# Performance work log

Measured on AMD Instinct MI355X. Metric: run time of the kernel, lower is better.

## Reference

```python
import jax, jax.numpy as jnp
import numpy as np
import math

B, T, D, H = 2, 2048, 1024, 16
HD = D // H


def setup_inputs() -> dict:
    key = jax.random.key(0)
    k1, k2, k3 = jax.random.split(key, 3)
    x = jax.random.normal(k1, (B, T, D), dtype=jnp.float32)
    # weights scaled like typical init to keep activations sane
    w_qkv = jax.random.normal(k2, (D, 3 * D), dtype=jnp.float32) / math.sqrt(D)
    w_out = jax.random.normal(k3, (D, D), dtype=jnp.float32) / math.sqrt(D)
    return {"x": x, "w_qkv": w_qkv, "w_out": w_out}


def reference(x, w_qkv, w_out):
    b, t, d = x.shape
    h, hd = H, HD
    qkv = x @ w_qkv                                # (b, t, 3d)
    qkv = qkv.reshape(b, t, h, 3 * hd).transpose(0, 2, 1, 3)  # (b, h, t, 3hd)
    q, k, v = jnp.split(qkv, 3, axis=-1)           # each (b, h, t, hd)
    scaled = jnp.einsum('bhqd,bhkd->bhqk', q, k) / math.sqrt(hd)
    # causal mask: strictly upper triangle -> -inf (as in torch.triu(full(-inf),1))
    causal = jnp.tril(jnp.ones((t, t), dtype=bool))
    scaled = jnp.where(causal, scaled, -jnp.inf)
    attn = jax.nn.softmax(scaled, axis=-1)
    vals = jnp.einsum('bhqk,bhkd->bhqd', attn, v)  # (b, h, t, hd)
    # NOTE: original reshapes (b,h,t,hd)->(b,t,h*hd) WITHOUT permuting heads back.
    vals = vals.reshape(b, t, h * hd)
    return vals @ w_out
```

## Files before the change

### kernel.cpp

```cpp
#include <hip/hip_runtime.h>
#include <hip/hip_bf16.h>
#include <math.h>

#define BB 2
#define TT 2048
#define DD 1024
#define HH 16
#define HDD 64

typedef __attribute__((ext_vector_type(8))) short short8;
typedef __attribute__((ext_vector_type(4))) float f32x4;

__device__ __forceinline__ short f2bf(float f) {
  __hip_bfloat16 h = __float2bfloat16(f);
  return *reinterpret_cast<short*>(&h);
}

__device__ __forceinline__ float bf2f(short s) {
  unsigned u = ((unsigned)(unsigned short)s) << 16;
  return __builtin_bit_cast(float, u);
}

__device__ __forceinline__ void gload_lds16(const void* g, void* l) {
  __builtin_amdgcn_global_load_lds(
      (const __attribute__((address_space(1))) unsigned int*)g,
      (__attribute__((address_space(3))) unsigned int*)l, 16, 0, 0);
}

__global__ __launch_bounds__(256) void cvt_f32_bf16(
    const float* __restrict__ in, short* __restrict__ out, int n8) {
  int i = blockIdx.x * 256 + threadIdx.x;
  if (i >= n8) return;
  const float4* p = (const float4*)in + (size_t)i * 2;
  float4 a = p[0], b = p[1];
  short8 o;
  o[0] = f2bf(a.x); o[1] = f2bf(a.y); o[2] = f2bf(a.z); o[3] = f2bf(a.w);
  o[4] = f2bf(b.x); o[5] = f2bf(b.y); o[6] = f2bf(b.z); o[7] = f2bf(b.w);
  *((short8*)out + i) = o;
}

__global__ __launch_bounds__(256) void transpose_f32_bf16(
    const float* __restrict__ W, short* __restrict__ WT, int R, int C) {
  __shared__ float tile[32][33];
  const int c0 = blockIdx.x * 32, r0 = blockIdx.y * 32;
  const int tx = threadIdx.x & 31, ty = threadIdx.x >> 5;
#pragma unroll
  for (int i = 0; i < 32; i += 8)
    tile[ty + i][tx] = W[(size_t)(r0 + ty + i) * C + c0 + tx];
  __syncthreads();
#pragma unroll
  for (int i = 0; i < 32; i += 8)
    WT[(size_t)(c0 + ty + i) * R + r0 + tx] = f2bf(tile[tx][ty + i]);
}

__global__ __launch_bounds__(256) void vtrans(const short* __restrict__ qkv,
                                              short* __restrict__ vtg) {
  const int t0 = blockIdx.x * 64;
  const int h = blockIdx.y, b = blockIdx.z;
  __shared__ __align__(16) short sm[64 * 64];
  const int tid = threadIdx.x;
  const short* Vg = qkv + (size_t)(b * TT) * 3072 + h * 192 + 128;
#pragma unroll
  for (int r2 = 0; r2 < 2; ++r2) {
    int c = tid + r2 * 256;
    int t = c >> 3, d0 = (c & 7) * 8;
    short8 v = *(const short8*)(Vg + (size_t)(t0 + t) * 3072 + d0);
#pragma unroll
    for (int j = 0; j < 8; ++j) {
      int d = d0 + j;
      int byte = (d << 7) + ((t * 2) ^ (((d >> 3) & 7) << 4));
      *(short*)((char*)sm + byte) = v[j];
    }
  }
  __syncthreads();
  short* outp = vtg + (size_t)(b * HH + h) * HDD * TT + t0;
#pragma unroll
  for (int r2 = 0; r2 < 2; ++r2) {
    int c = tid + r2 * 256;
    int d = c >> 3, tc = c & 7;
    int byte = (d << 7) + ((tc ^ ((d >> 3) & 7)) << 4);
    short8 v = *(const short8*)((char*)sm + byte);
    *(short8*)(outp + (size_t)d * TT + tc * 8) = v;
  }
}

template <bool OUT_BF16>
__global__ __launch_bounds__(256) void gemm_bf16_mfma(
    const short* __restrict__ A, const short* __restrict__ BT,
    void* __restrict__ Cv, int M, int N, int K) {
  constexpr int BM = 128, BN = 128, BK = 64;
  __shared__ __align__(16) short As[BM * BK];
  __shared__ __align__(16) short Bs[BN * BK];

  const int nbx = N / BN;
  const int nwg = nbx * (M / BM);
  int bid = blockIdx.x;
  {
    int q = nwg >> 3;
    bid = (bid & 7) * q + (bid >> 3);
  }
  const int m0 = (bid / nbx) * BM;
  const int n0 = (bid % nbx) * BN;

  const int tid = threadIdx.x;
  const int lane = tid & 63;
  const int l15 = lane & 15;
  const int g4 = lane >> 4;
  const int wm = tid >> 7;
  const int wn = (tid >> 6) & 1;
  const int swz = (l15 & 7) << 4;

  f32x4 acc[4][4];
#pragma unroll
  for (int i = 0; i < 4; ++i)
#pragma unroll
    for (int j = 0; j < 4; ++j) acc[i][j] = (f32x4){0.f, 0.f, 0.f, 0.f};

  for (int k0 = 0; k0 < K; k0 += BK) {
    __syncthreads();
#pragma unroll
    for (int r = 0; r < 4; ++r) {
      int c = tid + r * 256;
      int row = c >> 3, cc = c & 7;
      int sc = (cc ^ (row & 7)) * 8;
      gload_lds16(A + (size_t)(m0 + row) * K + k0 + sc, (char*)As + c * 16);
    }
#pragma unroll
    for (int r = 0; r < 4; ++r) {
      int c = tid + r * 256;
      int row = c >> 3, cc = c & 7;
      int sc = (cc ^ (row & 7)) * 8;
      gload_lds16(BT + (size_t)(n0 + row) * K + k0 + sc, (char*)Bs + c * 16);
    }
    __syncthreads();

#pragma unroll
    for (int kk = 0; kk < 2; ++kk) {
      short8 af[4], bfr[4];
#pragma unroll
      for (int i = 0; i < 4; ++i) {
        int row = wm * 64 + i * 16 + l15;
        af[i] = *(const short8*)((const char*)As + row * 128 +
                                 (((kk * 4 + g4) << 4) ^ swz));
      }
#pragma unroll
      for (int j = 0; j < 4; ++j) {
        int row = wn * 64 + j * 16 + l15;
        bfr[j] = *(const short8*)((const char*)Bs + row * 128 +
                                  (((kk * 4 + g4) << 4) ^ swz));
      }
#pragma unroll
      for (int i = 0; i < 4; ++i)
#pragma unroll
        for (int j = 0; j < 4; ++j)
          acc[i][j] = __builtin_amdgcn_mfma_f32_16x16x32_bf16(
              af[i], bfr[j], acc[i][j], 0, 0, 0);
    }
  }

#pragma unroll
  for (int i = 0; i < 4; ++i) {
#pragma unroll
    for (int j = 0; j < 4; ++j) {
#pragma unroll
      for (int r = 0; r < 4; ++r) {
        size_t idx = (size_t)(m0 + wm * 64 + i * 16 + g4 * 4 + r) * N +
                     n0 + wn * 64 + j * 16 + l15;
        if (OUT_BF16)
          ((short*)Cv)[idx] = f2bf(acc[i][j][r]);
        else
          ((float*)Cv)[idx] = acc[i][j][r];
      }
    }
  }
}

__global__ __launch_bounds__(256) void attn_flash4(
    const short* __restrict__ qkv, const short* __restrict__ vtg,
    short* __restrict__ vals, char* __restrict__ parts,
    float* __restrict__ mldiag) {
  const int bid = blockIdx.x;
  const int xcd = bid & 7;
  const int j   = bid >> 3;
  const int g   = xcd + ((j & 3) << 3);
  const int c   = 79 - (j >> 2);
  int qt, ci, cnt;
  if (c < 8)       { qt = c;                          ci = 0;      cnt = 1; }
  else if (c < 24) { int u = c - 8;  qt = 8 + (u >> 1);  ci = u & 1;  cnt = 2; }
  else if (c < 48) { int u = c - 24; qt = 16 + u / 3;    ci = u % 3;  cnt = 3; }
  else             { int u = c - 48; qt = 24 + (u >> 2); ci = u & 3;  cnt = 4; }
  const int h = g & 15, b = g >> 4;
  const int nt  = qt + 1;
  const int it0 = ci * 8;
  const int it1 = min(it0 + 8, nt);

  const int tid = threadIdx.x;
  const int w = tid >> 6, lane = tid & 63, l15 = lane & 15, g4 = lane >> 4;

  __shared__ __align__(16) short Ks[2][64 * 64];
  __shared__ __align__(16) short Vs[2][64 * 64];
  __shared__ __align__(16) short Ps[4 * 16 * 64];

  const size_t bhbase = (size_t)(b * TT) * 3072 + (size_t)h * 192;
  char* const pswb = (char*)Ps + w * 2048;

  const float MFIX = 12.0f;
  const float SSC = 0.18033688011112042f;

  const int c2 = tid + 256;
  const int r1 = tid >> 3, s1 = tid & 7;
  const int r2 = c2 >> 3,  s2 = c2 & 7;
  const size_t kgo1 = (size_t)r1 * 3072 + ((s1 ^ (r1 & 7)) * 8);
  const size_t kgo2 = (size_t)r2 * 3072 + ((s2 ^ (r2 & 7)) * 8);
  const size_t vgo1 = (size_t)r1 * TT + ((s1 ^ (r1 & 7)) * 8);
  const size_t vgo2 = (size_t)r2 * TT + ((s2 ^ (r2 & 7)) * 8);
  char* const ldsK0 = (char*)Ks[0] + tid * 16;
  char* const ldsK1 = (char*)Ks[1] + tid * 16;
  char* const ldsV0 = (char*)Vs[0] + tid * 16;
  char* const ldsV1 = (char*)Vs[1] + tid * 16;

  const short* kptr = qkv + bhbase + 64 + (size_t)(it0 * 64) * 3072;
  const short* vptr = vtg + (size_t)(b * HH + h) * HDD * TT + it0 * 64;

  auto STAGE = [&](int buf) {
    char* kl = buf ? ldsK1 : ldsK0;
    char* vl = buf ? ldsV1 : ldsV0;
    gload_lds16(kptr + kgo1, kl);
    gload_lds16(kptr + kgo2, kl + 4096);
    gload_lds16(vptr + vgo1, vl);
    gload_lds16(vptr + vgo2, vl + 4096);
    kptr += 64 * 3072;
    vptr += 64;
  };

  short8 qf0, qf1;
  {
    const int qrow = qt * 64 + w * 16 + l15;
    const short* Qp = qkv + bhbase + (size_t)qrow * 3072 + g4 * 8;
    short8 q0 = *(const short8*)(Qp);
    short8 q1 = *(const short8*)(Qp + 32);
#pragma unroll
    for (int jj = 0; jj < 8; ++jj) {
      qf0[jj] = f2bf(bf2f(q0[jj]) * SSC);
      qf1[jj] = f2bf(bf2f(q1[jj]) * SSC);
    }
  }

  float lsum = 0.f;
  f32x4 oacc[4];
#pragma unroll
  for (int dt = 0; dt < 4; ++dt) oacc[dt] = (f32x4){0.f, 0.f, 0.f, 0.f};

  STAGE(0);
  int cur = 0;

  const int pxor = (l15 & 3) << 1;
  const int sw = l15 & 7;

#pragma unroll 1
  for (int it = it0; it < it1; ++it) {
    __syncthreads();
    if (it + 1 < it1) STAGE(cur ^ 1);

    const char* ksb = cur ? (const char*)Ks[1] : (const char*)Ks[0];
    const char* vsb = cur ? (const char*)Vs[1] : (const char*)Vs[0];

    f32x4 s4[4];
    __builtin_amdgcn_s_setprio(1);
#pragma unroll
    for (int kt = 0; kt < 4; ++kt) {
      const char* kb = ksb + (kt * 16 + l15) * 128;
      short8 kf0 = *(const short8*)(kb + ((g4 ^ sw) << 4));
      short8 kf1 = *(const short8*)(kb + (((g4 + 4) ^ sw) << 4));
      s4[kt] = (f32x4){0.f, 0.f, 0.f, 0.f};
      s4[kt] = __builtin_amdgcn_mfma_f32_16x16x32_bf16(kf0, qf0, s4[kt], 0, 0, 0);
      s4[kt] = __builtin_amdgcn_mfma_f32_16x16x32_bf16(kf1, qf1, s4[kt], 0, 0, 0);
    }
    __builtin_amdgcn_s_setprio(0);

    if (it == qt) {
      const int qg = w * 16 + l15;
#pragma unroll
      for (int kt = 0; kt < 4; ++kt) {
#pragma unroll
        for (int r = 0; r < 4; ++r) {
          int kg = kt * 16 + g4 * 4 + r;
          if (kg > qg) s4[kt][r] = -INFINITY;
        }
      }
    }

    float p[4][4];
    float ts = 0.f;
#pragma unroll
    for (int kt = 0; kt < 4; ++kt)
#pragma unroll
      for (int r = 0; r < 4; ++r) {
        float e = exp2f(s4[kt][r] - MFIX);
        p[kt][r] = e;
        ts += e;
      }
    lsum += ts;

#pragma unroll
    for (int kt = 0; kt < 4; ++kt) {
      unsigned lo, hi;
      asm("v_cvt_pk_bf16_f32 %0, %1, %2" : "=v"(lo) : "v"(p[kt][0]), "v"(p[kt][1]));
      asm("v_cvt_pk_bf16_f32 %0, %1, %2" : "=v"(hi) : "v"(p[kt][2]), "v"(p[kt][3]));
      int slot = 2 * kt + (g4 >> 1);
      *(uint2*)(pswb + l15 * 128 + ((slot ^ pxor) << 4) + ((g4 & 1) << 3)) =
          make_uint2(lo, hi);
    }
    short8 pa0 = *(const short8*)(pswb + l15 * 128 + ((g4 ^ pxor) << 4));
    short8 pa1 = *(const short8*)(pswb + l15 * 128 + (((4 + g4) ^ pxor) << 4));

    __builtin_amdgcn_s_setprio(1);
#pragma unroll
    for (int dt = 0; dt < 4; ++dt) {
      const char* vb = vsb + (dt * 16 + l15) * 128;
      short8 vb0 = *(const short8*)(vb + ((g4 ^ sw) << 4));
      short8 vb1 = *(const short8*)(vb + (((g4 + 4) ^ sw) << 4));
      oacc[dt] = __builtin_amdgcn_mfma_f32_16x16x32_bf16(pa0, vb0, oacc[dt], 0, 0, 0);
      oacc[dt] = __builtin_amdgcn_mfma_f32_16x16x32_bf16(pa1, vb1, oacc[dt], 0, 0, 0);
    }
    __builtin_amdgcn_s_setprio(0);

    cur ^= 1;
  }

  lsum += __shfl_xor(lsum, 16);
  lsum += __shfl_xor(lsum, 32);

  if (cnt == 1) {
    float inv = 1.f / lsum;
    float invq[4];
#pragma unroll
    for (int r = 0; r < 4; ++r) invq[r] = __shfl(inv, g4 * 4 + r, 16);
#pragma unroll
    for (int r = 0; r < 4; ++r) {
      int qglob = qt * 64 + w * 16 + g4 * 4 + r;
      size_t rowbase = (((size_t)b * HH + h) * TT + qglob) * HDD;
#pragma unroll
      for (int dt = 0; dt < 4; ++dt)
        vals[rowbase + dt * 16 + l15] = f2bf(oacc[dt][r] * invq[r]);
    }
  } else if (ci == cnt - 1) {
#pragma unroll
    for (int r = 0; r < 4; ++r) {
      int qglob = qt * 64 + w * 16 + g4 * 4 + r;
      size_t rowbase = (((size_t)b * HH + h) * TT + qglob) * HDD;
#pragma unroll
      for (int dt = 0; dt < 4; ++dt)
        vals[rowbase + dt * 16 + l15] = f2bf(oacc[dt][r]);
    }
    if (g4 == 0) {
      int qtglob = g * 32 + qt;
      int qrow = w * 16 + l15;
      mldiag[qtglob * 128 + qrow] = MFIX;
      mldiag[qtglob * 128 + 64 + qrow] = lsum;
    }
  } else {
    int pl = (qt < 16) ? (qt - 8)
             : (qt < 24 ? 8 + (qt - 16) * 2 : 24 + (qt - 24) * 3);
    char* pp = parts + (size_t)(g * 48 + pl + ci) * 8704;
    short* po = (short*)pp;
#pragma unroll
    for (int r = 0; r < 4; ++r)
#pragma unroll
      for (int dt = 0; dt < 4; ++dt)
        po[(w * 16 + g4 * 4 + r) * 64 + dt * 16 + l15] = f2bf(oacc[dt][r]);
    if (g4 == 0) {
      int qrow = w * 16 + l15;
      *(float*)(pp + 8192 + qrow * 4) = MFIX;
      *(float*)(pp + 8448 + qrow * 4) = lsum;
    }
  }
}

__global__ __launch_bounds__(256) void attn_merge(
    short* __restrict__ vals, const char* __restrict__ parts,
    const float* __restrict__ mldiag) {
  const int qt = 8 + blockIdx.x;
  const int g  = blockIdx.y;
  const int tid = threadIdx.x;
  const int q  = tid >> 2;
  const int dq = (tid & 3) * 16;
  const int np = qt < 16 ? 1 : (qt < 24 ? 2 : 3);
  const int pl = (qt < 16) ? (qt - 8)
                 : (qt < 24 ? 8 + (qt - 16) * 2 : 24 + (qt - 24) * 3);
  const int qtglob = g * 32 + qt;
  const char* pbase = parts + (size_t)(g * 48 + pl) * 8704;

  float mdiag = mldiag[qtglob * 128 + q];
  float ldiag = mldiag[qtglob * 128 + 64 + q];

  float mstar = mdiag;
  for (int p = 0; p < np; ++p)
    mstar = fmaxf(mstar, *(const float*)(pbase + (size_t)p * 8704 + 8192 + q * 4));

  size_t vbase = ((size_t)g * TT + qt * 64 + q) * HDD + dq;
  float o[16];
  {
    float wd = exp2f(mdiag - mstar);
    short8 a = *(const short8*)(vals + vbase);
    short8 bb = *(const short8*)(vals + vbase + 8);
#pragma unroll
    for (int jj = 0; jj < 8; ++jj) {
      o[jj] = bf2f(a[jj]) * wd;
      o[8 + jj] = bf2f(bb[jj]) * wd;
    }
    ldiag *= wd;
  }
  float lacc = ldiag;
  for (int p = 0; p < np; ++p) {
    const char* pp = pbase + (size_t)p * 8704;
    float wp = exp2f(*(const float*)(pp + 8192 + q * 4) - mstar);
    lacc += *(const float*)(pp + 8448 + q * 4) * wp;
    const short* po = (const short*)pp + q * 64 + dq;
    short8 a = *(const short8*)po;
    short8 bb = *(const short8*)(po + 8);
#pragma unroll
    for (int jj = 0; jj < 8; ++jj) {
      o[jj] += bf2f(a[jj]) * wp;
      o[8 + jj] += bf2f(bb[jj]) * wp;
    }
  }
  float inv = 1.f / lacc;
  short8 oa, ob;
#pragma unroll
  for (int jj = 0; jj < 8; ++jj) {
    oa[jj] = f2bf(o[jj] * inv);
    ob[jj] = f2bf(o[8 + jj] * inv);
  }
  *(short8*)(vals + vbase) = oa;
  *(short8*)(vals + vbase + 8) = ob;
}

extern "C" void kernel_launch(void* const* d_in, const int* in_sizes, int n_in,
                              void* d_out, int out_size, void* d_ws, size_t ws_size,
                              hipStream_t stream) {
  const float* x     = (const float*)d_in[0];
  const float* w_qkv = (const float*)d_in[1];
  const float* w_out = (const float*)d_in[2];
  float* out = (float*)d_out;

  char* ws = (char*)d_ws;
  short* qkvb  = (short*)(ws);
  short* valsb = (short*)(ws + 25165824);
  short* xb    = (short*)(ws + 33554432);
  short* wqkvT = (short*)(ws + 41943040);
  short* woutT = (short*)(ws + 48234496);
  short* vtg   = (short*)(ws + 50331648);
  char*  parts = ws + 33554432;
  float* mldiag = (float*)(ws + 58720256);

  const int M = BB * TT;

  cvt_f32_bf16<<<(M * DD / 8 + 255) / 256, 256, 0, stream>>>(x, xb, M * DD / 8);
  {
    dim3 g(3 * DD / 32, DD / 32);
    transpose_f32_bf16<<<g, 256, 0, stream>>>(w_qkv, wqkvT, DD, 3 * DD);
  }
  {
    dim3 g(DD / 32, DD / 32);
    transpose_f32_bf16<<<g, 256, 0, stream>>>(w_out, woutT, DD, DD);
  }

  gemm_bf16_mfma<true><<<(M / 128) * (3 * DD / 128), 256, 0, stream>>>(
      xb, wqkvT, qkvb, M, 3 * DD, DD);

  {
    dim3 g(TT / 64, HH, BB);
    vtrans<<<g, 256, 0, stream>>>(qkvb, vtg);
  }

  attn_flash4<<<2560, 256, 0, stream>>>(qkvb, vtg, valsb, parts, mldiag);
  {
    dim3 g(24, 32);
    attn_merge<<<g, 256, 0, stream>>>(valsb, parts, mldiag);
  }

  gemm_bf16_mfma<false><<<(M / 128) * (DD / 128), 256, 0, stream>>>(
      valsb, woutT, out, M, DD, DD);
}
```

Before: 120.9 us.

## Process paired query tiles per attention block and merge prep kernels

The attention kernel now has each block handle two adjacent 64-row query tiles, so every K/V tile staged in LDS is reused by both. The causal work split is rebalanced to a new triangular chunking with 2304 blocks, and the partial-result buffers are enlarged and spill into the output buffer. The merge kernel is rewritten to match. The three prep kernels (x conversion and the two weight transposes) are fused into one launch to cut launch overhead. The risks are higher register pressure from the doubled accumulators and a tricky new partition and indexing scheme that reuses the output buffer as scratch.

```diff
diff --git a/kernel.cpp b/kernel.cpp
--- a/kernel.cpp
+++ b/kernel.cpp
@@ -11,6 +11,9 @@
 typedef __attribute__((ext_vector_type(8))) short short8;
 typedef __attribute__((ext_vector_type(4))) float f32x4;
 
+#define PART_SPLIT 843
+#define PART_BYTES 17408
+
 __device__ __forceinline__ short f2bf(float f) {
   __hip_bfloat16 h = __float2bfloat16(f);
   return *reinterpret_cast<short*>(&h);
@@ -27,23 +30,37 @@
       (__attribute__((address_space(3))) unsigned int*)l, 16, 0, 0);
 }
 
-__global__ __launch_bounds__(256) void cvt_f32_bf16(
-    const float* __restrict__ in, short* __restrict__ out, int n8) {
-  int i = blockIdx.x * 256 + threadIdx.x;
-  if (i >= n8) return;
-  const float4* p = (const float4*)in + (size_t)i * 2;
-  float4 a = p[0], b = p[1];
-  short8 o;
-  o[0] = f2bf(a.x); o[1] = f2bf(a.y); o[2] = f2bf(a.z); o[3] = f2bf(a.w);
-  o[4] = f2bf(b.x); o[5] = f2bf(b.y); o[6] = f2bf(b.z); o[7] = f2bf(b.w);
-  *((short8*)out + i) = o;
-}
-
-__global__ __launch_bounds__(256) void transpose_f32_bf16(
-    const float* __restrict__ W, short* __restrict__ WT, int R, int C) {
+__global__ __launch_bounds__(256) void prep(
+    const float* __restrict__ x, const float* __restrict__ w_qkv,
+    const float* __restrict__ w_out, short* __restrict__ xb,
+    short* __restrict__ wqkvT, short* __restrict__ woutT) {
   __shared__ float tile[32][33];
-  const int c0 = blockIdx.x * 32, r0 = blockIdx.y * 32;
-  const int tx = threadIdx.x & 31, ty = threadIdx.x >> 5;
+  const int bid = blockIdx.x;
+  const int tid = threadIdx.x;
+  if (bid < 2048) {
+    int i = bid * 256 + tid;
+    const float4* pp = (const float4*)x + (size_t)i * 2;
+    float4 a = pp[0], bq = pp[1];
+    short8 o;
+    o[0] = f2bf(a.x); o[1] = f2bf(a.y); o[2] = f2bf(a.z); o[3] = f2bf(a.w);
+    o[4] = f2bf(bq.x); o[5] = f2bf(bq.y); o[6] = f2bf(bq.z); o[7] = f2bf(bq.w);
+    *((short8*)xb + i) = o;
+    return;
+  }
+  const float* W;
+  short* WT;
+  int R, C, bx, by;
+  if (bid < 2048 + 3072) {
+    int t = bid - 2048;
+    bx = t % 96; by = t / 96;
+    W = w_qkv; WT = wqkvT; R = 1024; C = 3072;
+  } else {
+    int t = bid - 5120;
+    bx = t & 31; by = t >> 5;
+    W = w_out; WT = woutT; R = 1024; C = 1024;
+  }
+  const int c0 = bx * 32, r0 = by * 32;
+  const int tx = tid & 31, ty = tid >> 5;
 #pragma unroll
   for (int i = 0; i < 32; i += 8)
     tile[ty + i][tx] = W[(size_t)(r0 + ty + i) * C + c0 + tx];
@@ -175,24 +192,26 @@
   }
 }
 
-__global__ __launch_bounds__(256) void attn_flash4(
+__global__ __launch_bounds__(256) void attn_flash5(
     const short* __restrict__ qkv, const short* __restrict__ vtg,
-    short* __restrict__ vals, char* __restrict__ parts,
-    float* __restrict__ mldiag) {
+    short* __restrict__ vals, char* __restrict__ partsA,
+    char* __restrict__ partsB, float* __restrict__ mldiag) {
   const int bid = blockIdx.x;
   const int xcd = bid & 7;
   const int j   = bid >> 3;
   const int g   = xcd + ((j & 3) << 3);
-  const int c   = 79 - (j >> 2);
-  int qt, ci, cnt;
-  if (c < 8)       { qt = c;                          ci = 0;      cnt = 1; }
-  else if (c < 24) { int u = c - 8;  qt = 8 + (u >> 1);  ci = u & 1;  cnt = 2; }
-  else if (c < 48) { int u = c - 24; qt = 16 + u / 3;    ci = u % 3;  cnt = 3; }
-  else             { int u = c - 48; qt = 24 + (u >> 2); ci = u & 3;  cnt = 4; }
+  const int c   = 71 - (j >> 2);
+  int k = 0;
+  while ((k + 1) * (k + 2) <= c) ++k;
+  const int u   = c - k * (k + 1);
+  const int dlt = (u >= k + 1) ? 1 : 0;
+  const int p   = 2 * k + dlt;
+  const int ci  = u - dlt * (k + 1);
+  const int cnt = k + 1;
   const int h = g & 15, b = g >> 4;
-  const int nt  = qt + 1;
-  const int it0 = ci * 8;
-  const int it1 = min(it0 + 8, nt);
+  const int nt  = 2 * p + 2;
+  const int it0 = ci * nt / cnt;
+  const int it1 = (ci + 1) * nt / cnt;
 
   const int tid = threadIdx.x;
   const int w = tid >> 6, lane = tid & 63, l15 = lane & 15, g4 = lane >> 4;
@@ -233,27 +252,33 @@
     vptr += 64;
   };
 
-  short8 qf0, qf1;
+  short8 qf00, qf01, qf10, qf11;
   {
-    const int qrow = qt * 64 + w * 16 + l15;
-    const short* Qp = qkv + bhbase + (size_t)qrow * 3072 + g4 * 8;
-    short8 q0 = *(const short8*)(Qp);
-    short8 q1 = *(const short8*)(Qp + 32);
+    const short* Qp0 = qkv + bhbase + (size_t)(p * 128 + w * 16 + l15) * 3072 + g4 * 8;
+    const short* Qp1 = Qp0 + (size_t)64 * 3072;
+    short8 a0 = *(const short8*)(Qp0);
+    short8 a1 = *(const short8*)(Qp0 + 32);
+    short8 b0 = *(const short8*)(Qp1);
+    short8 b1 = *(const short8*)(Qp1 + 32);
 #pragma unroll
     for (int jj = 0; jj < 8; ++jj) {
-      qf0[jj] = f2bf(bf2f(q0[jj]) * SSC);
-      qf1[jj] = f2bf(bf2f(q1[jj]) * SSC);
-    }
-  }
-
-  float lsum = 0.f;
-  f32x4 oacc[4];
-#pragma unroll
-  for (int dt = 0; dt < 4; ++dt) oacc[dt] = (f32x4){0.f, 0.f, 0.f, 0.f};
+      qf00[jj] = f2bf(bf2f(a0[jj]) * SSC);
+      qf01[jj] = f2bf(bf2f(a1[jj]) * SSC);
+      qf10[jj] = f2bf(bf2f(b0[jj]) * SSC);
+      qf11[jj] = f2bf(bf2f(b1[jj]) * SSC);
+    }
+  }
+
+  float lsum0 = 0.f, lsum1 = 0.f;
+  f32x4 oacc0[4], oacc1[4];
+#pragma unroll
+  for (int dt = 0; dt < 4; ++dt) {
+    oacc0[dt] = (f32x4){0.f, 0.f, 0.f, 0.f};
+    oacc1[dt] = (f32x4){0.f, 0.f, 0.f, 0.f};
+  }
 
   STAGE(0);
   int cur = 0;
-
   const int pxor = (l15 & 3) << 1;
   const int sw = l15 & 7;
 
@@ -264,55 +289,91 @@
 
     const char* ksb = cur ? (const char*)Ks[1] : (const char*)Ks[0];
     const char* vsb = cur ? (const char*)Vs[1] : (const char*)Vs[0];
-
-    f32x4 s4[4];
+    const bool a0 = (it <= 2 * p);
+
+    f32x4 s0[4], s1[4];
     __builtin_amdgcn_s_setprio(1);
 #pragma unroll
     for (int kt = 0; kt < 4; ++kt) {
       const char* kb = ksb + (kt * 16 + l15) * 128;
       short8 kf0 = *(const short8*)(kb + ((g4 ^ sw) << 4));
       short8 kf1 = *(const short8*)(kb + (((g4 + 4) ^ sw) << 4));
-      s4[kt] = (f32x4){0.f, 0.f, 0.f, 0.f};
-      s4[kt] = __builtin_amdgcn_mfma_f32_16x16x32_bf16(kf0, qf0, s4[kt], 0, 0, 0);
-      s4[kt] = __builtin_amdgcn_mfma_f32_16x16x32_bf16(kf1, qf1, s4[kt], 0, 0, 0);
+      if (a0) {
+        s0[kt] = (f32x4){0.f, 0.f, 0.f, 0.f};
+        s0[kt] = __builtin_amdgcn_mfma_f32_16x16x32_bf16(kf0, qf00, s0[kt], 0, 0, 0);
+        s0[kt] = __builtin_amdgcn_mfma_f32_16x16x32_bf16(kf1, qf01, s0[kt], 0, 0, 0);
+      }
+      s1[kt] = (f32x4){0.f, 0.f, 0.f, 0.f};
+      s1[kt] = __builtin_amdgcn_mfma_f32_16x16x32_bf16(kf0, qf10, s1[kt], 0, 0, 0);
+      s1[kt] = __builtin_amdgcn_mfma_f32_16x16x32_bf16(kf1, qf11, s1[kt], 0, 0, 0);
     }
     __builtin_amdgcn_s_setprio(0);
 
-    if (it == qt) {
-      const int qg = w * 16 + l15;
+    const int qg = w * 16 + l15;
+    if (it == 2 * p) {
+#pragma unroll
+      for (int kt = 0; kt < 4; ++kt)
+#pragma unroll
+        for (int r = 0; r < 4; ++r)
+          if (kt * 16 + g4 * 4 + r > qg) s0[kt][r] = -INFINITY;
+    }
+    if (it == 2 * p + 1) {
+#pragma unroll
+      for (int kt = 0; kt < 4; ++kt)
+#pragma unroll
+        for (int r = 0; r < 4; ++r)
+          if (kt * 16 + g4 * 4 + r > qg) s1[kt][r] = -INFINITY;
+    }
+
+    short8 paA0, paA1, paB0, paB1;
+    if (a0) {
+      float ts = 0.f;
+      float pq[4][4];
+#pragma unroll
+      for (int kt = 0; kt < 4; ++kt)
+#pragma unroll
+        for (int r = 0; r < 4; ++r) {
+          float e = exp2f(s0[kt][r] - MFIX);
+          pq[kt][r] = e;
+          ts += e;
+        }
+      lsum0 += ts;
 #pragma unroll
       for (int kt = 0; kt < 4; ++kt) {
+        unsigned lo, hi;
+        asm("v_cvt_pk_bf16_f32 %0, %1, %2" : "=v"(lo) : "v"(pq[kt][0]), "v"(pq[kt][1]));
+        asm("v_cvt_pk_bf16_f32 %0, %1, %2" : "=v"(hi) : "v"(pq[kt][2]), "v"(pq[kt][3]));
+        int slot = 2 * kt + (g4 >> 1);
+        *(uint2*)(pswb + l15 * 128 + ((slot ^ pxor) << 4) + ((g4 & 1) << 3)) =
+            make_uint2(lo, hi);
+      }
+      paA0 = *(const short8*)(pswb + l15 * 128 + ((g4 ^ pxor) << 4));
+      paA1 = *(const short8*)(pswb + l15 * 128 + (((4 + g4) ^ pxor) << 4));
+    }
+    {
+      float ts = 0.f;
+      float pq[4][4];
+#pragma unroll
+      for (int kt = 0; kt < 4; ++kt)
 #pragma unroll
         for (int r = 0; r < 4; ++r) {
-          int kg = kt * 16 + g4 * 4 + r;
-          if (kg > qg) s4[kt][r] = -INFINITY;
+          float e = exp2f(s1[kt][r] - MFIX);
+          pq[kt][r] = e;
+          ts += e;
         }
-      }
-    }
-
-    float p[4][4];
-    float ts = 0.f;
-#pragma unroll
-    for (int kt = 0; kt < 4; ++kt)
-#pragma unroll
-      for (int r = 0; r < 4; ++r) {
-        float e = exp2f(s4[kt][r] - MFIX);
-        p[kt][r] = e;
-        ts += e;
-      }
-    lsum += ts;
-
-#pragma unroll
-    for (int kt = 0; kt < 4; ++kt) {
-      unsigned lo, hi;
-      asm("v_cvt_pk_bf16_f32 %0, %1, %2" : "=v"(lo) : "v"(p[kt][0]), "v"(p[kt][1]));
-      asm("v_cvt_pk_bf16_f32 %0, %1, %2" : "=v"(hi) : "v"(p[kt][2]), "v"(p[kt][3]));
-      int slot = 2 * kt + (g4 >> 1);
-      *(uint2*)(pswb + l15 * 128 + ((slot ^ pxor) << 4) + ((g4 & 1) << 3)) =
-          make_uint2(lo, hi);
-    }
-    short8 pa0 = *(const short8*)(pswb + l15 * 128 + ((g4 ^ pxor) << 4));
-    short8 pa1 = *(const short8*)(pswb + l15 * 128 + (((4 + g4) ^ pxor) << 4));
+      lsum1 += ts;
+#pragma unroll
+      for (int kt = 0; kt < 4; ++kt) {
+        unsigned lo, hi;
+        asm("v_cvt_pk_bf16_f32 %0, %1, %2" : "=v"(lo) : "v"(pq[kt][0]), "v"(pq[kt][1]));
+        asm("v_cvt_pk_bf16_f32 %0, %1, %2" : "=v"(hi) : "v"(pq[kt][2]), "v"(pq[kt][3]));
+        int slot = 2 * kt + (g4 >> 1);
+        *(uint2*)(pswb + l15 * 128 + ((slot ^ pxor) << 4) + ((g4 & 1) << 3)) =
+            make_uint2(lo, hi);
+      }
+      paB0 = *(const short8*)(pswb + l15 * 128 + ((g4 ^ pxor) << 4));
+      paB1 = *(const short8*)(pswb + l15 * 128 + (((4 + g4) ^ pxor) << 4));
+    }
 
     __builtin_amdgcn_s_setprio(1);
 #pragma unroll
@@ -320,120 +381,163 @@
       const char* vb = vsb + (dt * 16 + l15) * 128;
       short8 vb0 = *(const short8*)(vb + ((g4 ^ sw) << 4));
       short8 vb1 = *(const short8*)(vb + (((g4 + 4) ^ sw) << 4));
-      oacc[dt] = __builtin_amdgcn_mfma_f32_16x16x32_bf16(pa0, vb0, oacc[dt], 0, 0, 0);
-      oacc[dt] = __builtin_amdgcn_mfma_f32_16x16x32_bf16(pa1, vb1, oacc[dt], 0, 0, 0);
+      if (a0) {
+        oacc0[dt] = __builtin_amdgcn_mfma_f32_16x16x32_bf16(paA0, vb0, oacc0[dt], 0, 0, 0);
+        oacc0[dt] = __builtin_amdgcn_mfma_f32_16x16x32_bf16(paA1, vb1, oacc0[dt], 0, 0, 0);
+      }
+      oacc1[dt] = __builtin_amdgcn_mfma_f32_16x16x32_bf16(paB0, vb0, oacc1[dt], 0, 0, 0);
+      oacc1[dt] = __builtin_amdgcn_mfma_f32_16x16x32_bf16(paB1, vb1, oacc1[dt], 0, 0, 0);
     }
     __builtin_amdgcn_s_setprio(0);
 
     cur ^= 1;
   }
 
-  lsum += __shfl_xor(lsum, 16);
-  lsum += __shfl_xor(lsum, 32);
-
+  lsum0 += __shfl_xor(lsum0, 16);
+  lsum0 += __shfl_xor(lsum0, 32);
+  lsum1 += __shfl_xor(lsum1, 16);
+  lsum1 += __shfl_xor(lsum1, 32);
+
+  const size_t vrow0 = (size_t)g * TT + p * 128 + w * 16;
   if (cnt == 1) {
-    float inv = 1.f / lsum;
-    float invq[4];
-#pragma unroll
-    for (int r = 0; r < 4; ++r) invq[r] = __shfl(inv, g4 * 4 + r, 16);
+    float inv0 = 1.f / lsum0, inv1 = 1.f / lsum1;
+    float i0q[4], i1q[4];
 #pragma unroll
     for (int r = 0; r < 4; ++r) {
-      int qglob = qt * 64 + w * 16 + g4 * 4 + r;
-      size_t rowbase = (((size_t)b * HH + h) * TT + qglob) * HDD;
-#pragma unroll
-      for (int dt = 0; dt < 4; ++dt)
-        vals[rowbase + dt * 16 + l15] = f2bf(oacc[dt][r] * invq[r]);
+      i0q[r] = __shfl(inv0, g4 * 4 + r, 16);
+      i1q[r] = __shfl(inv1, g4 * 4 + r, 16);
+    }
+#pragma unroll
+    for (int r = 0; r < 4; ++r) {
+      size_t rb0 = (vrow0 + g4 * 4 + r) * HDD;
+      size_t rb1 = (vrow0 + 64 + g4 * 4 + r) * HDD;
+#pragma unroll
+      for (int dt = 0; dt < 4; ++dt) {
+        vals[rb0 + dt * 16 + l15] = f2bf(oacc0[dt][r] * i0q[r]);
+        vals[rb1 + dt * 16 + l15] = f2bf(oacc1[dt][r] * i1q[r]);
+      }
     }
   } else if (ci == cnt - 1) {
 #pragma unroll
     for (int r = 0; r < 4; ++r) {
-      int qglob = qt * 64 + w * 16 + g4 * 4 + r;
-      size_t rowbase = (((size_t)b * HH + h) * TT + qglob) * HDD;
-#pragma unroll
-      for (int dt = 0; dt < 4; ++dt)
-        vals[rowbase + dt * 16 + l15] = f2bf(oacc[dt][r]);
+      size_t rb0 = (vrow0 + g4 * 4 + r) * HDD;
+      size_t rb1 = (vrow0 + 64 + g4 * 4 + r) * HDD;
+#pragma unroll
+      for (int dt = 0; dt < 4; ++dt) {
+        vals[rb0 + dt * 16 + l15] = f2bf(oacc0[dt][r]);
+        vals[rb1 + dt * 16 + l15] = f2bf(oacc1[dt][r]);
+      }
     }
     if (g4 == 0) {
-      int qtglob = g * 32 + qt;
-      int qrow = w * 16 + l15;
-      mldiag[qtglob * 128 + qrow] = MFIX;
-      mldiag[qtglob * 128 + 64 + qrow] = lsum;
+      int base = (g * 16 + p) * 256;
+      int qr = w * 16 + l15;
+      mldiag[base + qr] = MFIX;
+      mldiag[base + 64 + qr] = MFIX;
+      mldiag[base + 128 + qr] = lsum0;
+      mldiag[base + 192 + qr] = lsum1;
     }
   } else {
-    int pl = (qt < 16) ? (qt - 8)
-             : (qt < 24 ? 8 + (qt - 16) * 2 : 24 + (qt - 24) * 3);
-    char* pp = parts + (size_t)(g * 48 + pl + ci) * 8704;
+    const int PL = k * (k - 1) + dlt * k;
+    const int e = g * 56 + PL + ci;
+    char* pp = (e < PART_SPLIT) ? (partsA + (size_t)e * PART_BYTES)
+                                : (partsB + (size_t)(e - PART_SPLIT) * PART_BYTES);
     short* po = (short*)pp;
 #pragma unroll
-    for (int r = 0; r < 4; ++r)
-#pragma unroll
-      for (int dt = 0; dt < 4; ++dt)
-        po[(w * 16 + g4 * 4 + r) * 64 + dt * 16 + l15] = f2bf(oacc[dt][r]);
+    for (int r = 0; r < 4; ++r) {
+      int rr0 = w * 16 + g4 * 4 + r;
+#pragma unroll
+      for (int dt = 0; dt < 4; ++dt) {
+        po[rr0 * 64 + dt * 16 + l15] = f2bf(oacc0[dt][r]);
+        po[(64 + rr0) * 64 + dt * 16 + l15] = f2bf(oacc1[dt][r]);
+      }
+    }
     if (g4 == 0) {
-      int qrow = w * 16 + l15;
-      *(float*)(pp + 8192 + qrow * 4) = MFIX;
-      *(float*)(pp + 8448 + qrow * 4) = lsum;
-    }
-  }
-}
-
-__global__ __launch_bounds__(256) void attn_merge(
-    short* __restrict__ vals, const char* __restrict__ parts,
-    const float* __restrict__ mldiag) {
-  const int qt = 8 + blockIdx.x;
-  const int g  = blockIdx.y;
+      int qr = w * 16 + l15;
+      *(float*)(pp + 16384 + qr * 4) = MFIX;
+      *(float*)(pp + 16384 + (64 + qr) * 4) = MFIX;
+      *(float*)(pp + 16896 + qr * 4) = lsum0;
+      *(float*)(pp + 16896 + (64 + qr) * 4) = lsum1;
+    }
+  }
+}
+
+__global__ __launch_bounds__(256) void attn_merge2(
+    short* __restrict__ vals, const char* __restrict__ partsA,
+    const char* __restrict__ partsB, const float* __restrict__ mldiag) {
+  const int p = 2 + blockIdx.x;
+  const int g = blockIdx.y;
+  const int k = p >> 1, dlt = p & 1;
+  const int np = k;
+  const int PL = k * (k - 1) + dlt * k;
+  const int e0 = g * 56 + PL;
   const int tid = threadIdx.x;
-  const int q  = tid >> 2;
-  const int dq = (tid & 3) * 16;
-  const int np = qt < 16 ? 1 : (qt < 24 ? 2 : 3);
-  const int pl = (qt < 16) ? (qt - 8)
-                 : (qt < 24 ? 8 + (qt - 16) * 2 : 24 + (qt - 24) * 3);
-  const int qtglob = g * 32 + qt;
-  const char* pbase = parts + (size_t)(g * 48 + pl) * 8704;
-
-  float mdiag = mldiag[qtglob * 128 + q];
-  float ldiag = mldiag[qtglob * 128 + 64 + q];
+  const int row = tid >> 1;
+  const int dh = (tid & 1) << 5;
+  const int base = (g * 16 + p) * 256;
+
+  float mdiag = mldiag[base + row];
+  float ldiag = mldiag[base + 128 + row];
 
   float mstar = mdiag;
-  for (int p = 0; p < np; ++p)
-    mstar = fmaxf(mstar, *(const float*)(pbase + (size_t)p * 8704 + 8192 + q * 4));
-
-  size_t vbase = ((size_t)g * TT + qt * 64 + q) * HDD + dq;
-  float o[16];
+  for (int e = 0; e < np; ++e) {
+    int ee = e0 + e;
+    const char* pp = (ee < PART_SPLIT)
+                         ? (partsA + (size_t)ee * PART_BYTES)
+                         : (partsB + (size_t)(ee - PART_SPLIT) * PART_BYTES);
+    mstar = fmaxf(mstar, *(const float*)(pp + 16384 + row * 4));
+  }
+
+  size_t vbase = ((size_t)g * TT + p * 128 + row) * HDD + dh;
+  float o[32];
   {
     float wd = exp2f(mdiag - mstar);
-    short8 a = *(const short8*)(vals + vbase);
-    short8 bb = *(const short8*)(vals + vbase + 8);
+    short8 v0 = *(const short8*)(vals + vbase);
+    short8 v1 = *(const short8*)(vals + vbase + 8);
+    short8 v2 = *(const short8*)(vals + vbase + 16);
+    short8 v3 = *(const short8*)(vals + vbase + 24);
 #pragma unroll
     for (int jj = 0; jj < 8; ++jj) {
-      o[jj] = bf2f(a[jj]) * wd;
-      o[8 + jj] = bf2f(bb[jj]) * wd;
+      o[jj] = bf2f(v0[jj]) * wd;
+      o[8 + jj] = bf2f(v1[jj]) * wd;
+      o[16 + jj] = bf2f(v2[jj]) * wd;
+      o[24 + jj] = bf2f(v3[jj]) * wd;
     }
     ldiag *= wd;
   }
   float lacc = ldiag;
-  for (int p = 0; p < np; ++p) {
-    const char* pp = pbase + (size_t)p * 8704;
-    float wp = exp2f(*(const float*)(pp + 8192 + q * 4) - mstar);
-    lacc += *(const float*)(pp + 8448 + q * 4) * wp;
-    const short* po = (const short*)pp + q * 64 + dq;
-    short8 a = *(const short8*)po;
-    short8 bb = *(const short8*)(po + 8);
+  for (int e = 0; e < np; ++e) {
+    int ee = e0 + e;
+    const char* pp = (ee < PART_SPLIT)
+                         ? (partsA + (size_t)ee * PART_BYTES)
+                         : (partsB + (size_t)(ee - PART_SPLIT) * PART_BYTES);
+    float wp = exp2f(*(const float*)(pp + 16384 + row * 4) - mstar);
+    lacc += *(const float*)(pp + 16896 + row * 4) * wp;
+    const short* po = (const short*)pp + row * 64 + dh;
+    short8 v0 = *(const short8*)po;
+    short8 v1 = *(const short8*)(po + 8);
+    short8 v2 = *(const short8*)(po + 16);
+    short8 v3 = *(const short8*)(po + 24);
 #pragma unroll
     for (int jj = 0; jj < 8; ++jj) {
-      o[jj] += bf2f(a[jj]) * wp;
-      o[8 + jj] += bf2f(bb[jj]) * wp;
+      o[jj] += bf2f(v0[jj]) * wp;
+      o[8 + jj] += bf2f(v1[jj]) * wp;
+      o[16 + jj] += bf2f(v2[jj]) * wp;
+      o[24 + jj] += bf2f(v3[jj]) * wp;
     }
   }
   float inv = 1.f / lacc;
-  short8 oa, ob;
+  short8 w0, w1, w2, w3;
 #pragma unroll
   for (int jj = 0; jj < 8; ++jj) {
-    oa[jj] = f2bf(o[jj] * inv);
-    ob[jj] = f2bf(o[8 + jj] * inv);
-  }
-  *(short8*)(vals + vbase) = oa;
-  *(short8*)(vals + vbase + 8) = ob;
+    w0[jj] = f2bf(o[jj] * inv);
+    w1[jj] = f2bf(o[8 + jj] * inv);
+    w2[jj] = f2bf(o[16 + jj] * inv);
+    w3[jj] = f2bf(o[24 + jj] * inv);
+  }
+  *(short8*)(vals + vbase) = w0;
+  *(short8*)(vals + vbase + 8) = w1;
+  *(short8*)(vals + vbase + 16) = w2;
+  *(short8*)(vals + vbase + 24) = w3;
 }
 
 extern "C" void kernel_launch(void* const* d_in, const int* in_sizes, int n_in,
@@ -451,20 +555,13 @@
   short* wqkvT = (short*)(ws + 41943040);
   short* woutT = (short*)(ws + 48234496);
   short* vtg   = (short*)(ws + 50331648);
-  char*  parts = ws + 33554432;
+  char*  partsA = ws + 33554432;
+  char*  partsB = (char*)d_out;
   float* mldiag = (float*)(ws + 58720256);
 
   const int M = BB * TT;
 
-  cvt_f32_bf16<<<(M * DD / 8 + 255) / 256, 256, 0, stream>>>(x, xb, M * DD / 8);
-  {
-    dim3 g(3 * DD / 32, DD / 32);
-    transpose_f32_bf16<<<g, 256, 0, stream>>>(w_qkv, wqkvT, DD, 3 * DD);
-  }
-  {
-    dim3 g(DD / 32, DD / 32);
-    transpose_f32_bf16<<<g, 256, 0, stream>>>(w_out, woutT, DD, DD);
-  }
+  prep<<<6144, 256, 0, stream>>>(x, w_qkv, w_out, xb, wqkvT, woutT);
 
   gemm_bf16_mfma<true><<<(M / 128) * (3 * DD / 128), 256, 0, stream>>>(
       xb, wqkvT, qkvb, M, 3 * DD, DD);
@@ -474,10 +571,10 @@
     vtrans<<<g, 256, 0, stream>>>(qkvb, vtg);
   }
 
-  attn_flash4<<<2560, 256, 0, stream>>>(qkvb, vtg, valsb, parts, mldiag);
+  attn_flash5<<<2304, 256, 0, stream>>>(qkvb, vtg, valsb, partsA, partsB, mldiag);
   {
-    dim3 g(24, 32);
-    attn_merge<<<g, 256, 0, stream>>>(valsb, parts, mldiag);
+    dim3 g(14, 32);
+    attn_merge2<<<g, 256, 0, stream>>>(valsb, partsA, partsB, mldiag);
   }
 
   gemm_bf16_mfma<false><<<(M / 128) * (DD / 128), 256, 0, stream>>>(
```

New measurement: 164.6 us. 1.36x slower.
